# Kernel tuning notes

Measured on AMD Instinct MI355X. Metric: run time of the kernel, lower is better.

## Reference

```python
import jax, jax.numpy as jnp
import numpy as np

K = 3  # kernel size
PAD = K // 2


def setup_inputs() -> dict:
    key = jax.random.key(0)
    k1, k2, k3 = jax.random.split(key, 3)
    B, C, H, W = 8, 192, 128, 128
    x = jax.random.normal(k1, (B, C, H, W), dtype=jnp.float32)
    kernel = 0.02 * jax.random.normal(k2, (C, K * K), dtype=jnp.float32)
    gate_w = 0.02 * jax.random.normal(k3, (C,), dtype=jnp.float32)
    gate_b = jnp.zeros((C,), dtype=jnp.float32)
    return {"x": x, "kernel": kernel, "gate_w": gate_w, "gate_b": gate_b}


def reference(x, kernel, gate_w, gate_b):
    B, C, H, W = x.shape
    # F.unfold with zero padding: patches[b,c,ki*K+kj,h,w] = x_pad[b,c,h+ki,w+kj]
    xp = jnp.pad(x, ((0, 0), (0, 0), (PAD, PAD), (PAD, PAD)))
    patches = jnp.stack(
        [xp[:, :, i:i + H, j:j + W] for i in range(K) for j in range(K)],
        axis=2,
    )  # [B, C, K*K, H, W]
    # depthwise 1x1 gate: per-channel scale + bias, then sigmoid
    theta = jax.nn.sigmoid(x * gate_w[None, :, None, None] + gate_b[None, :, None, None])
    # max-plus: max_v [ f(u-v) + theta(u) * k(v) ]
    scored = patches + theta[:, :, None] * kernel[None, :, :, None, None]
    return jnp.max(scored, axis=2)  # [B, C, H, W]
```

## Files before the change

### kernel.cpp

```cpp
#include <hip/hip_runtime.h>
#include <math.h>

#define BB 8
#define CC 192
#define HH 128
#define WW 128
#define NV4   (BB * CC * HH * WW / 4)
#define NBLK  2048
#define NTHR  (NBLK * 256)
#define NIT   (NV4 / NTHR)


typedef float vf4 __attribute__((ext_vector_type(4)));

__device__ __forceinline__ float col9(float a0, float a1, float a2,
                                      float b0, float b1, float b2,
                                      float c0, float c1, float c2,
                                      float th, const float* kk) {
    float m;
    m = fmaf(th, kk[0], a0);
    m = fmaxf(m, fmaf(th, kk[1], a1));
    m = fmaxf(m, fmaf(th, kk[2], a2));
    m = fmaxf(m, fmaf(th, kk[3], b0));
    m = fmaxf(m, fmaf(th, kk[4], b1));
    m = fmaxf(m, fmaf(th, kk[5], b2));
    m = fmaxf(m, fmaf(th, kk[6], c0));
    m = fmaxf(m, fmaf(th, kk[7], c1));
    m = fmaxf(m, fmaf(th, kk[8], c2));
    return m;
}

__global__ __launch_bounds__(256) void dynmorph_kernel(
    const float* __restrict__ x,
    const float* __restrict__ kern,
    const float* __restrict__ gw,
    const float* __restrict__ gb,
    float* __restrict__ out)
{
    const int tid  = threadIdx.x;
    const int lane = tid & 63;
    const int wg   = lane & 31;

    int i = blockIdx.x * 256 + tid;

#pragma unroll
    for (int k = 0; k < NIT; ++k, i += NTHR) {
        const int c = __builtin_amdgcn_readfirstlane((i >> 12) % CC);
        const int r = (i >> 5) & (HH - 1);

        float kk[9];
#pragma unroll
        for (int q = 0; q < 9; ++q) kk[q] = kern[c * 9 + q];
        const float gwc = gw[c];
        const float gbc = gb[c];

        const float* p = x + ((size_t)i << 2);
        const vf4 Bv = *(const vf4*)p;
        const vf4 A  = (r > 0)      ? *(const vf4*)(p - WW) : (vf4)(0.0f);
        const vf4 Cv = (r < HH - 1) ? *(const vf4*)(p + WW) : (vf4)(0.0f);

        const float aL0 = __shfl_up(A.w, 1),  aR0 = __shfl_down(A.x, 1);
        const float bL0 = __shfl_up(Bv.w, 1), bR0 = __shfl_down(Bv.x, 1);
        const float cL0 = __shfl_up(Cv.w, 1), cR0 = __shfl_down(Cv.x, 1);
        const float aL = (wg == 0)  ? 0.0f : aL0;
        const float bL = (wg == 0)  ? 0.0f : bL0;
        const float cL = (wg == 0)  ? 0.0f : cL0;
        const float aR = (wg == 31) ? 0.0f : aR0;
        const float bR = (wg == 31) ? 0.0f : bR0;
        const float cR = (wg == 31) ? 0.0f : cR0;

        const float t0 = __builtin_amdgcn_rcpf(1.0f + __expf(-fmaf(Bv.x, gwc, gbc)));
        const float t1 = __builtin_amdgcn_rcpf(1.0f + __expf(-fmaf(Bv.y, gwc, gbc)));
        const float t2 = __builtin_amdgcn_rcpf(1.0f + __expf(-fmaf(Bv.z, gwc, gbc)));
        const float t3 = __builtin_amdgcn_rcpf(1.0f + __expf(-fmaf(Bv.w, gwc, gbc)));

        vf4 o;
        o.x = col9(aL,   A.x,  A.y,
                   bL,   Bv.x, Bv.y,
                   cL,   Cv.x, Cv.y, t0, kk);
        o.y = col9(A.x,  A.y,  A.z,
                   Bv.x, Bv.y, Bv.z,
                   Cv.x, Cv.y, Cv.z, t1, kk);
        o.z = col9(A.y,  A.z,  A.w,
                   Bv.y, Bv.z, Bv.w,
                   Cv.y, Cv.z, Cv.w, t2, kk);
        o.w = col9(A.z,  A.w,  aR,
                   Bv.z, Bv.w, bR,
                   Cv.z, Cv.w, cR, t3, kk);

        *(vf4*)(out + ((size_t)i << 2)) = o;
    }
}

extern "C" void kernel_launch(void* const* d_in, const int* in_sizes, int n_in,
                              void* d_out, int out_size, void* d_ws, size_t ws_size,
                              hipStream_t stream) {
    const float* x    = (const float*)d_in[0];
    const float* kern = (const float*)d_in[1];
    const float* gw   = (const float*)d_in[2];
    const float* gb   = (const float*)d_in[3];
    float* out        = (float*)d_out;

    dim3 grid(NBLK);
    dim3 block(256);
    dynmorph_kernel<<<grid, block, 0, stream>>>(x, kern, gw, gb, out);
}
```

Baseline: 182.9 us.

## Stage row bands with halos in shared memory to avoid triple global loads

Each block now handles a 16-row band of one (batch, channel) plane. It loads the band plus one halo row above and below into LDS, then reads the neighbouring rows from LDS instead of issuing three global loads per element. This cuts redundant global and L2 traffic and moves per-channel parameter loads out of the loop. In exchange it adds a barrier, extra halo loads for 2 of every 18 rows, and loses the grid-stride loop, launching many more small blocks.

```diff
diff --git a/kernel.cpp b/kernel.cpp
--- a/kernel.cpp
+++ b/kernel.cpp
@@ -5,10 +5,10 @@
 #define CC 192
 #define HH 128
 #define WW 128
-#define NV4   (BB * CC * HH * WW / 4)
-#define NBLK  2048
-#define NTHR  (NBLK * 256)
-#define NIT   (NV4 / NTHR)
+#define BANDR 16
+#define NBANDS (HH / BANDR)
+#define NBLK  (BB * CC * NBANDS)
+#define LROWS (BANDR + 2)
 
 
 typedef float vf4 __attribute__((ext_vector_type(4)));
@@ -30,66 +30,88 @@
     return m;
 }
 
-__global__ __launch_bounds__(256) void dynmorph_kernel(
+__global__ __launch_bounds__(512) void dynmorph_kernel(
     const float* __restrict__ x,
     const float* __restrict__ kern,
     const float* __restrict__ gw,
     const float* __restrict__ gb,
     float* __restrict__ out)
 {
+    __shared__ float sm[LROWS * WW];
+
     const int tid  = threadIdx.x;
-    const int lane = tid & 63;
-    const int wg   = lane & 31;
+    const int wg   = tid & 31;
+    const int col  = wg * 4;
+    const int lrow = tid >> 5;
 
-    int i = blockIdx.x * 256 + tid;
+    const int blk  = blockIdx.x;
+    const int bc   = blk >> 3;
+    const int band = blk & 7;
+    const int c    = bc % CC;
+    const int r0   = band * BANDR;
 
+    const float* xb = x   + (size_t)bc * (HH * WW);
+    float*       ob = out + (size_t)bc * (HH * WW);
+
+    const int gr = r0 + lrow;
+    const vf4 Bv = *(const vf4*)(xb + gr * WW + col);
+
+    vf4 hv = (vf4)(0.0f);
+    int hvalid = 0, hldsr = 0;
+    if (tid < 64) {
+        const int hrow = (tid < 32) ? (r0 - 1) : (r0 + BANDR);
+        const int clmp = hrow < 0 ? 0 : (hrow > HH - 1 ? HH - 1 : hrow);
+        hv     = *(const vf4*)(xb + clmp * WW + (tid & 31) * 4);
+        hvalid = (hrow >= 0 && hrow < HH);
+        hldsr  = (tid < 32) ? 0 : (LROWS - 1);
+    }
+
+    float kk[9];
 #pragma unroll
-    for (int k = 0; k < NIT; ++k, i += NTHR) {
-        const int c = __builtin_amdgcn_readfirstlane((i >> 12) % CC);
-        const int r = (i >> 5) & (HH - 1);
+    for (int q = 0; q < 9; ++q) kk[q] = kern[c * 9 + q];
+    const float gwc = gw[c];
+    const float gbc = gb[c];
 
-        float kk[9];
-#pragma unroll
-        for (int q = 0; q < 9; ++q) kk[q] = kern[c * 9 + q];
-        const float gwc = gw[c];
-        const float gbc = gb[c];
+    *(vf4*)(&sm[(lrow + 1) * WW + col]) = Bv;
+    if (tid < 64) {
+        if (!hvalid) hv = (vf4)(0.0f);
+        *(vf4*)(&sm[hldsr * WW + (tid & 31) * 4]) = hv;
+    }
+    __syncthreads();
 
-        const float* p = x + ((size_t)i << 2);
-        const vf4 Bv = *(const vf4*)p;
-        const vf4 A  = (r > 0)      ? *(const vf4*)(p - WW) : (vf4)(0.0f);
-        const vf4 Cv = (r < HH - 1) ? *(const vf4*)(p + WW) : (vf4)(0.0f);
+    const vf4 A  = *(const vf4*)(&sm[lrow * WW + col]);
+    const vf4 Cv = *(const vf4*)(&sm[(lrow + 2) * WW + col]);
 
-        const float aL0 = __shfl_up(A.w, 1),  aR0 = __shfl_down(A.x, 1);
-        const float bL0 = __shfl_up(Bv.w, 1), bR0 = __shfl_down(Bv.x, 1);
-        const float cL0 = __shfl_up(Cv.w, 1), cR0 = __shfl_down(Cv.x, 1);
-        const float aL = (wg == 0)  ? 0.0f : aL0;
-        const float bL = (wg == 0)  ? 0.0f : bL0;
-        const float cL = (wg == 0)  ? 0.0f : cL0;
-        const float aR = (wg == 31) ? 0.0f : aR0;
-        const float bR = (wg == 31) ? 0.0f : bR0;
-        const float cR = (wg == 31) ? 0.0f : cR0;
+    const float aL0 = __shfl_up(A.w, 1),  aR0 = __shfl_down(A.x, 1);
+    const float bL0 = __shfl_up(Bv.w, 1), bR0 = __shfl_down(Bv.x, 1);
+    const float cL0 = __shfl_up(Cv.w, 1), cR0 = __shfl_down(Cv.x, 1);
+    const float aL = (wg == 0)  ? 0.0f : aL0;
+    const float bL = (wg == 0)  ? 0.0f : bL0;
+    const float cL = (wg == 0)  ? 0.0f : cL0;
+    const float aR = (wg == 31) ? 0.0f : aR0;
+    const float bR = (wg == 31) ? 0.0f : bR0;
+    const float cR = (wg == 31) ? 0.0f : cR0;
 
-        const float t0 = __builtin_amdgcn_rcpf(1.0f + __expf(-fmaf(Bv.x, gwc, gbc)));
-        const float t1 = __builtin_amdgcn_rcpf(1.0f + __expf(-fmaf(Bv.y, gwc, gbc)));
-        const float t2 = __builtin_amdgcn_rcpf(1.0f + __expf(-fmaf(Bv.z, gwc, gbc)));
-        const float t3 = __builtin_amdgcn_rcpf(1.0f + __expf(-fmaf(Bv.w, gwc, gbc)));
+    const float t0 = __builtin_amdgcn_rcpf(1.0f + __expf(-fmaf(Bv.x, gwc, gbc)));
+    const float t1 = __builtin_amdgcn_rcpf(1.0f + __expf(-fmaf(Bv.y, gwc, gbc)));
+    const float t2 = __builtin_amdgcn_rcpf(1.0f + __expf(-fmaf(Bv.z, gwc, gbc)));
+    const float t3 = __builtin_amdgcn_rcpf(1.0f + __expf(-fmaf(Bv.w, gwc, gbc)));
 
-        vf4 o;
-        o.x = col9(aL,   A.x,  A.y,
-                   bL,   Bv.x, Bv.y,
-                   cL,   Cv.x, Cv.y, t0, kk);
-        o.y = col9(A.x,  A.y,  A.z,
-                   Bv.x, Bv.y, Bv.z,
-                   Cv.x, Cv.y, Cv.z, t1, kk);
-        o.z = col9(A.y,  A.z,  A.w,
-                   Bv.y, Bv.z, Bv.w,
-                   Cv.y, Cv.z, Cv.w, t2, kk);
-        o.w = col9(A.z,  A.w,  aR,
-                   Bv.z, Bv.w, bR,
-                   Cv.z, Cv.w, cR, t3, kk);
+    vf4 o;
+    o.x = col9(aL,   A.x,  A.y,
+               bL,   Bv.x, Bv.y,
+               cL,   Cv.x, Cv.y, t0, kk);
+    o.y = col9(A.x,  A.y,  A.z,
+               Bv.x, Bv.y, Bv.z,
+               Cv.x, Cv.y, Cv.z, t1, kk);
+    o.z = col9(A.y,  A.z,  A.w,
+               Bv.y, Bv.z, Bv.w,
+               Cv.y, Cv.z, Cv.w, t2, kk);
+    o.w = col9(A.z,  A.w,  aR,
+               Bv.z, Bv.w, bR,
+               Cv.z, Cv.w, cR, t3, kk);
 
-        *(vf4*)(out + ((size_t)i << 2)) = o;
-    }
+    *(vf4*)(ob + gr * WW + col) = o;
 }
 
 extern "C" void kernel_launch(void* const* d_in, const int* in_sizes, int n_in,
@@ -102,6 +124,6 @@
     float* out        = (float*)d_out;
 
     dim3 grid(NBLK);
-    dim3 block(256);
+    dim3 block(512);
     dynmorph_kernel<<<grid, block, 0, stream>>>(x, kern, gw, gb, out);
 }
```

Measured after the change: 176.0 us. 3.8% less time.

## Process two rows per wave and share the middle row via cross-half shuffles

Applied to the files above, without the earlier changes.

Each wave now handles a pair of adjacent rows, one per 32-lane half. Each lane loads its own row plus one outer halo row, and gets the remaining neighbour row from the other half through lane shuffles instead of a third global load. This cuts global loads per output from three rows to two, at the cost of extra shuffle instructions and selects. The work mapping also changes to contiguous per-wave row pairs within a channel plane.

```diff
diff --git a/kernel.cpp b/kernel.cpp
--- a/kernel.cpp
+++ b/kernel.cpp
@@ -5,10 +5,10 @@
 #define CC 192
 #define HH 128
 #define WW 128
-#define NV4   (BB * CC * HH * WW / 4)
+#define NUNIT (BB * CC * (HH / 2))
 #define NBLK  2048
-#define NTHR  (NBLK * 256)
-#define NIT   (NV4 / NTHR)
+#define NWAVES (NBLK * 4)
+#define NIT   (NUNIT / NWAVES)
 
 
 typedef float vf4 __attribute__((ext_vector_type(4)));
@@ -40,13 +40,19 @@
     const int tid  = threadIdx.x;
     const int lane = tid & 63;
     const int wg   = lane & 31;
-
-    int i = blockIdx.x * 256 + tid;
+    const int hf   = lane >> 5;
+    const int col  = wg * 4;
+    const int wid  = __builtin_amdgcn_readfirstlane(blockIdx.x * 4 + (tid >> 6));
 
 #pragma unroll
-    for (int k = 0; k < NIT; ++k, i += NTHR) {
-        const int c = __builtin_amdgcn_readfirstlane((i >> 12) % CC);
-        const int r = (i >> 5) & (HH - 1);
+    for (int k = 0; k < NIT; ++k) {
+        const int u  = k * NWAVES + wid;
+        const int bc = u >> 6;
+        const int r  = (u & 63) * 2;
+        const int c  = bc % CC;
+
+        const float* xb = x   + (size_t)bc * (HH * WW);
+        float*       ob = out + (size_t)bc * (HH * WW);
 
         float kk[9];
 #pragma unroll
@@ -54,20 +60,31 @@
         const float gwc = gw[c];
         const float gbc = gb[c];
 
-        const float* p = x + ((size_t)i << 2);
-        const vf4 Bv = *(const vf4*)p;
-        const vf4 A  = (r > 0)      ? *(const vf4*)(p - WW) : (vf4)(0.0f);
-        const vf4 Cv = (r < HH - 1) ? *(const vf4*)(p + WW) : (vf4)(0.0f);
+        const int rc = r + hf;
+        const vf4 Bv = *(const vf4*)(xb + rc * WW + col);
 
-        const float aL0 = __shfl_up(A.w, 1),  aR0 = __shfl_down(A.x, 1);
-        const float bL0 = __shfl_up(Bv.w, 1), bR0 = __shfl_down(Bv.x, 1);
-        const float cL0 = __shfl_up(Cv.w, 1), cR0 = __shfl_down(Cv.x, 1);
-        const float aL = (wg == 0)  ? 0.0f : aL0;
-        const float bL = (wg == 0)  ? 0.0f : bL0;
-        const float cL = (wg == 0)  ? 0.0f : cL0;
-        const float aR = (wg == 31) ? 0.0f : aR0;
-        const float bR = (wg == 31) ? 0.0f : bR0;
-        const float cR = (wg == 31) ? 0.0f : cR0;
+        const int ro  = hf ? (r + 2) : (r - 1);
+        const int roc = ro < 0 ? 0 : (ro > HH - 1 ? HH - 1 : ro);
+        vf4 Ov = *(const vf4*)(xb + roc * WW + col);
+        const int oval = hf ? (ro < HH) : (ro >= 0);
+        if (!oval) Ov = (vf4)(0.0f);
+
+        float bl = __shfl_up(Bv.w, 1), br = __shfl_down(Bv.x, 1);
+        bl = (wg == 0) ? 0.0f : bl;  br = (wg == 31) ? 0.0f : br;
+        float ol = __shfl_up(Ov.w, 1), orr = __shfl_down(Ov.x, 1);
+        ol = (wg == 0) ? 0.0f : ol;  orr = (wg == 31) ? 0.0f : orr;
+
+        const int sl = lane ^ 32;
+        vf4 Sv;
+        Sv.x = __shfl(Bv.x, sl); Sv.y = __shfl(Bv.y, sl);
+        Sv.z = __shfl(Bv.z, sl); Sv.w = __shfl(Bv.w, sl);
+        const float slh = __shfl(bl, sl);
+        const float srh = __shfl(br, sl);
+
+        const vf4   A  = hf ? Sv  : Ov;
+        const vf4   Cv = hf ? Ov  : Sv;
+        const float aL = hf ? slh : ol,  aR = hf ? srh : orr;
+        const float cL = hf ? ol  : slh, cR = hf ? orr : srh;
 
         const float t0 = __builtin_amdgcn_rcpf(1.0f + __expf(-fmaf(Bv.x, gwc, gbc)));
         const float t1 = __builtin_amdgcn_rcpf(1.0f + __expf(-fmaf(Bv.y, gwc, gbc)));
@@ -76,7 +93,7 @@
 
         vf4 o;
         o.x = col9(aL,   A.x,  A.y,
-                   bL,   Bv.x, Bv.y,
+                   bl,   Bv.x, Bv.y,
                    cL,   Cv.x, Cv.y, t0, kk);
         o.y = col9(A.x,  A.y,  A.z,
                    Bv.x, Bv.y, Bv.z,
@@ -85,10 +102,10 @@
                    Bv.y, Bv.z, Bv.w,
                    Cv.y, Cv.z, Cv.w, t2, kk);
         o.w = col9(A.z,  A.w,  aR,
-                   Bv.z, Bv.w, bR,
+                   Bv.z, Bv.w, br,
                    Cv.z, Cv.w, cR, t3, kk);
 
-        *(vf4*)(out + ((size_t)i << 2)) = o;
+        *(vf4*)(ob + rc * WW + col) = o;
     }
 }
 
```

Result: no change. 180.4 us (-1.4%).
